# Kernel tuning notes

Measured on AMD Instinct MI355X. Metric: run time of the kernel, lower is better.

The kernel has to match this reference:

```python
import jax, jax.numpy as jnp
import numpy as np

WS = 8          # window_size
SHIFT = 4       # shift_size
HEADS = 12
C = 384
HD = C // HEADS
SCALE = HD ** -0.5
N = WS * WS


def _rel_pos_index(Wh, Ww):
    # double_step_seq(2*Ww-1, Wh, 1, Ww) -> (1, Wh*Ww); idx = rel + rel.T; flip along axis 1
    seq1 = np.arange(0, (2 * Ww - 1) * Wh, 2 * Ww - 1)
    seq2 = np.arange(0, Ww)
    rel = (seq1[:, None] + seq2[None, :]).reshape(1, -1)
    idx = rel + rel.T
    return np.flip(idx, 1).copy()

REL_IDX = jnp.asarray(_rel_pos_index(WS, WS))  # [N, N] int


def window_partition(x, ws):
    # x: [B, H, W, C] -> [B*nW, ws*ws, C]
    B, H, W, Cc = x.shape
    x = x.reshape(B, H // ws, ws, W // ws, ws, Cc).transpose(0, 1, 3, 2, 4, 5)
    return x.reshape(-1, ws * ws, Cc)


def window_reverse(win, H, W, ws):
    B = win.shape[0] // ((H // ws) * (W // ws))
    x = win.reshape(B, H // ws, W // ws, ws, ws, -1).transpose(0, 1, 3, 2, 4, 5)
    return x.reshape(B, H, W, -1)


def _attn_mask(H, W, ws, shift):
    # region ids 0..8 per (h,w) as in the torch slice loop
    hi = np.arange(H)
    wi = np.arange(W)
    h_id = (hi >= H - ws).astype(np.int32) + (hi >= H - shift).astype(np.int32)
    w_id = (wi >= W - ws).astype(np.int32) + (wi >= W - shift).astype(np.int32)
    cnt = (h_id[:, None] * 3 + w_id[None, :]).astype(np.float32)
    img = jnp.asarray(cnt)[None, :, :, None]              # [1, H, W, 1]
    mw = window_partition(img, ws).reshape(-1, ws * ws)   # [nW, N]
    diff = mw[:, None, :] - mw[:, :, None]                # [nW, N, N]
    return jnp.where(diff != 0, jnp.float32(-100.0), jnp.float32(0.0))


def setup_inputs() -> dict:
    key = jax.random.key(0)
    ks = jax.random.split(key, 8)
    B, H, W = 16, 96, 96
    std = 0.02
    return {
        "query": jax.random.normal(ks[0], (B, H * W, C), jnp.float32),
        "skip_query": jax.random.normal(ks[1], (B, H * W, C), jnp.float32),
        "W_qkv": jax.random.normal(ks[2], (C, 2 * C), jnp.float32) * std,
        "b_qkv": jnp.zeros((2 * C,), jnp.float32),
        "W_skip": jax.random.normal(ks[3], (C, C), jnp.float32) * std,
        "b_skip": jnp.zeros((C,), jnp.float32),
        "rpb_table": jax.random.normal(ks[4], ((2 * WS - 1) * (2 * WS - 1), HEADS), jnp.float32) * std,
        "W_proj": jax.random.normal(ks[5], (C, C), jnp.float32) * std,
        "b_proj": jnp.zeros((C,), jnp.float32),
        "h": H,
        "w": W,
    }


def reference(query, skip_query, W_qkv, b_qkv, W_skip, b_skip, rpb_table, W_proj, b_proj, h, w):
    B, L, Cc = query.shape
    q4 = query.reshape(B, h, w, Cc)
    s4 = skip_query.reshape(B, h, w, Cc)
    pad_r = (WS - w % WS) % WS
    pad_b = (WS - h % WS) % WS
    q4 = jnp.pad(q4, ((0, 0), (0, pad_b), (0, pad_r), (0, 0)))
    s4 = jnp.pad(s4, ((0, 0), (0, pad_b), (0, pad_r), (0, 0)))
    H_pad, W_pad = q4.shape[1], q4.shape[2]

    # cyclic shift
    q4 = jnp.roll(q4, (-SHIFT, -SHIFT), axis=(1, 2))
    s4 = jnp.roll(s4, (-SHIFT, -SHIFT), axis=(1, 2))
    mask = _attn_mask(H_pad, W_pad, WS, SHIFT)  # [nW, N, N]

    xw = window_partition(q4, WS)   # [Bn, N, C] -> k, v source
    sw = window_partition(s4, WS)   # [Bn, N, C] -> q source
    Bn = xw.shape[0]

    kv = (xw @ W_qkv + b_qkv).reshape(Bn, N, 2, HEADS, HD)
    k = kv[:, :, 0].transpose(0, 2, 1, 3)   # [Bn, H, N, d]
    v = kv[:, :, 1].transpose(0, 2, 1, 3)
    q = ((sw @ W_skip + b_skip).reshape(Bn, N, HEADS, HD).transpose(0, 2, 1, 3)) * SCALE

    attn = jnp.einsum('bhnd,bhmd->bhnm', q, k)  # [Bn, H, N, N]
    rpb = rpb_table[REL_IDX.reshape(-1)].reshape(N, N, HEADS).transpose(2, 0, 1)
    attn = attn + rpb[None]
    nW = mask.shape[0]
    attn = (attn.reshape(B, nW, HEADS, N, N) + mask[None, :, None]).reshape(Bn, HEADS, N, N)
    attn = jax.nn.softmax(attn, axis=-1)

    out = jnp.einsum('bhnm,bhmd->bhnd', attn, v).transpose(0, 2, 1, 3).reshape(Bn, N, Cc)
    out = out @ W_proj + b_proj

    x4 = window_reverse(out.reshape(-1, WS, WS, Cc), H_pad, W_pad, WS)
    x4 = jnp.roll(x4, (SHIFT, SHIFT), axis=(1, 2))
    x4 = x4[:, :h, :w]
    return x4.reshape(B, h * w, Cc)
```

## Files before the change

kernel.cpp:

```cpp
#include <hip/hip_runtime.h>
#include <hip/hip_bf16.h>


typedef __attribute__((ext_vector_type(8))) short short8;
typedef __attribute__((ext_vector_type(4))) float floatx4;

#define MFMA16(a, b, c) __builtin_amdgcn_mfma_f32_16x16x32_bf16(a, b, c, 0, 0, 0)

__device__ __forceinline__ short f2bf(float f) {
    __hip_bfloat16 h = __float2bfloat16(f);
    return *reinterpret_cast<short*>(&h);
}

__device__ __forceinline__ unsigned cvt2bf(float lo, float hi) {
    unsigned r;
    asm("v_cvt_pk_bf16_f32 %0, %1, %2" : "=v"(r) : "v"(lo), "v"(hi));
    return r;
}

__device__ __forceinline__ void glds16(const void* g, void* l) {
    __builtin_amdgcn_global_load_lds(
        (const __attribute__((address_space(1))) void*)g,
        (__attribute__((address_space(3))) void*)l, 16, 0, 0);
}


__global__ __launch_bounds__(256) void prep_wt(const float* __restrict__ Wqkv,
                                               const float* __restrict__ Wskip,
                                               short* __restrict__ Wt) {
    int tid = blockIdx.x * 256 + threadIdx.x;
    if (tid >= 384 * 144) return;
    int k = tid / 144;
    int n8 = (tid % 144) * 8;
#pragma unroll
    for (int e = 0; e < 8; e++) {
        int n = n8 + e;
        float v = (n < 768) ? Wqkv[k * 768 + n]
                            : Wskip[k * 384 + (n - 768)] * 0.17677669529663687f;
        Wt[(size_t)n * 384 + k] = f2bf(v);
    }
}

__global__ __launch_bounds__(256) void prep_wtp(const float* __restrict__ Wproj,
                                                short* __restrict__ WtP) {
    int tid = blockIdx.x * 256 + threadIdx.x;
    if (tid >= 384 * 48) return;
    int k = tid / 48;
    int n8 = (tid % 48) * 8;
#pragma unroll
    for (int e = 0; e < 8; e++) {
        int n = n8 + e;
        WtP[(size_t)n * 384 + k] = f2bf(Wproj[k * 384 + n]);
    }
}

__global__ __launch_bounds__(256) void prep_bias(const float* __restrict__ rpb,
                                                 float* __restrict__ bias64) {
    int tid = blockIdx.x * 256 + threadIdx.x;
    if (tid >= 49152) return;
    int h = tid >> 12;
    int rem = tid & 4095;
    int i = rem >> 6, kk = rem & 63;
    int j = 63 - kk;
    int ridx = 15 * (i >> 3) + (i & 7) + 15 * (j >> 3) + (j & 7);
    bias64[tid] = rpb[ridx * 12 + h];
}

template <bool SWP, bool FIN>
__device__ __forceinline__ void kloop12(
    const short* __restrict__ smemA, short* __restrict__ bwb,
    const short* __restrict__ curSrc, const short* __restrict__ nxtSrc,
    const int (&bso)[3], int l15, int g4, int al7, int brd,
    floatx4 (&acc)[3][4]) {
#pragma unroll
    for (int a = 0; a < 3; a++)
#pragma unroll
        for (int b = 0; b < 4; b++)
#pragma unroll
            for (int r = 0; r < 4; r++) acc[a][b][r] = 0.f;

#pragma unroll
    for (int kt = 0; kt < 12; ++kt) {
        if (FIN && kt == 11) {
            asm volatile("s_waitcnt vmcnt(0)" ::: "memory");
        } else {
            asm volatile("s_waitcnt vmcnt(3)" ::: "memory");
        }
        const int choff = ((kt * 4 + g4) ^ al7) * 8;
        short8 af[4], bfr[3];
#pragma unroll
        for (int b = 0; b < 4; b++)
            af[b] = *(const short8*)(smemA + (b * 16 + l15) * 384 + choff);
        short* hb = bwb + (kt & 1) * 1536;
#pragma unroll
        for (int nj = 0; nj < 3; nj++)
            bfr[nj] = *(const short8*)(hb + (nj * 16 + l15) * 32 + brd);
        __builtin_amdgcn_sched_barrier(0);
        asm volatile("s_waitcnt lgkmcnt(0)" ::: "memory");
        if (kt < 10) {
            int ko = (kt + 2) * 32;
#pragma unroll
            for (int j = 0; j < 3; j++)
                glds16(curSrc + bso[j] + ko, hb + j * 512);
        } else if (!FIN) {
            int ko = (kt - 10) * 32;
#pragma unroll
            for (int j = 0; j < 3; j++)
                glds16(nxtSrc + bso[j] + ko, hb + j * 512);
        }
        __builtin_amdgcn_sched_barrier(0);
        if (SWP) {
#pragma unroll
            for (int a = 0; a < 3; a++)
#pragma unroll
                for (int b = 0; b < 4; b++)
                    acc[a][b] = MFMA16(bfr[a], af[b], acc[a][b]);
        } else {
#pragma unroll
            for (int a = 0; a < 3; a++)
#pragma unroll
                for (int b = 0; b < 4; b++)
                    acc[a][b] = MFMA16(af[b], bfr[a], acc[a][b]);
        }
    }
}

__global__ __launch_bounds__(512, 1) void gemm_qkv(
    const float* __restrict__ xq, const float* __restrict__ xs,
    const short* __restrict__ Wt,
    const float* __restrict__ bqkv, const float* __restrict__ bskip,
    short* __restrict__ kbuf, short* __restrict__ vtbuf, short* __restrict__ qbuf) {
    __shared__ short smem[49152];

    const int win = blockIdx.x;
    const int var = blockIdx.y;
    const float* __restrict__ src = var ? xs : xq;

    const int tid = threadIdx.x, lane = tid & 63, wid = tid >> 6;
    const int l15 = lane & 15, g4 = lane >> 4;
    const int al7 = l15 & 7;
    const int brd = (g4 ^ ((l15 ^ (l15 >> 2)) & 3)) * 8;

    {
        int r = tid >> 3, q8 = tid & 7;
        int b = win / 144, wr = win % 144;
        int wy = wr / 12, wx = wr % 12;
        int yy = wy * 8 + (r >> 3) + 4; if (yy >= 96) yy -= 96;
        int xx = wx * 8 + (r & 7) + 4;  if (xx >= 96) xx -= 96;
        const float* rbase = src + ((size_t)b * 9216 + yy * 96 + xx) * 384;
        short* lrow = smem + r * 384;
        int r7 = r & 7;
#pragma unroll
        for (int j = 0; j < 6; j++) {
            int c = q8 + j * 8;
            float4 f0 = *(const float4*)(rbase + c * 8);
            float4 f1 = *(const float4*)(rbase + c * 8 + 4);
            uint4 u;
            u.x = cvt2bf(f0.x, f0.y); u.y = cvt2bf(f0.z, f0.w);
            u.z = cvt2bf(f1.x, f1.y); u.w = cvt2bf(f1.z, f1.w);
            *(uint4*)(lrow + ((c ^ r7) * 8)) = u;
        }
    }

    const int sw_st = ((lane >> 2) ^ (lane >> 4)) & 3;
    int bso[3];
#pragma unroll
    for (int j = 0; j < 3; j++)
        bso[j] = (j * 16 + (lane >> 2)) * 384 + (((lane & 3) ^ sw_st) * 8);
    short* bwb = smem + 24576 + wid * 3072;

    const short* src0 = Wt + (size_t)((var ? 768 : 0) + wid * 48) * 384;
    const short* src1 = Wt + (size_t)(384 + wid * 48) * 384;

#pragma unroll
    for (int j = 0; j < 3; j++) glds16(src0 + bso[j], bwb + j * 512);
#pragma unroll
    for (int j = 0; j < 3; j++) glds16(src0 + bso[j] + 32, bwb + 1536 + j * 512);
    __syncthreads();

    floatx4 acc[3][4];
    if (var == 0) {
        kloop12<true, false>(smem, bwb, src0, src1, bso, l15, g4, al7, brd, acc);
#pragma unroll
        for (int a = 0; a < 3; a++) {
            int nm = wid * 48 + a * 16 + g4 * 4;
            int head = nm >> 5, d0 = nm & 31;
            float4 bv = *(const float4*)(bqkv + nm);
            short* dst = kbuf + (size_t)(win * 12 + head) * 2048 + d0;
#pragma unroll
            for (int b = 0; b < 4; b++) {
                int t = b * 16 + l15;
                uint2 pk;
                pk.x = cvt2bf(acc[a][b][0] + bv.x, acc[a][b][1] + bv.y);
                pk.y = cvt2bf(acc[a][b][2] + bv.z, acc[a][b][3] + bv.w);
                *(uint2*)(dst + (size_t)t * 32) = pk;
            }
        }
        kloop12<false, true>(smem, bwb, src1, nullptr, bso, l15, g4, al7, brd, acc);
#pragma unroll
        for (int nj = 0; nj < 3; nj++) {
            int nm = wid * 48 + nj * 16 + l15;
            int head = nm >> 5, d = nm & 31;
            float bvs = bqkv[384 + nm];
            short* dst = vtbuf + ((size_t)(win * 12 + head) * 32 + d) * 64;
#pragma unroll
            for (int mi = 0; mi < 4; mi++) {
                int t0 = mi * 16 + g4 * 4;
                uint2 pk;
                pk.x = cvt2bf(acc[nj][mi][0] + bvs, acc[nj][mi][1] + bvs);
                pk.y = cvt2bf(acc[nj][mi][2] + bvs, acc[nj][mi][3] + bvs);
                *(uint2*)(dst + t0) = pk;
            }
        }
    } else {
        kloop12<true, true>(smem, bwb, src0, nullptr, bso, l15, g4, al7, brd, acc);
        const float scl = 0.17677669529663687f;
#pragma unroll
        for (int a = 0; a < 3; a++) {
            int nm = wid * 48 + a * 16 + g4 * 4;
            int head = nm >> 5, d0 = nm & 31;
            float4 bv = *(const float4*)(bskip + nm);
            short* dst = qbuf + (size_t)(win * 12 + head) * 2048 + d0;
#pragma unroll
            for (int b = 0; b < 4; b++) {
                int t = b * 16 + l15;
                uint2 pk;
                pk.x = cvt2bf(acc[a][b][0] + bv.x * scl, acc[a][b][1] + bv.y * scl);
                pk.y = cvt2bf(acc[a][b][2] + bv.z * scl, acc[a][b][3] + bv.w * scl);
                *(uint2*)(dst + (size_t)t * 32) = pk;
            }
        }
    }
}

__global__ __launch_bounds__(256) void attn_kernel(
    const short* __restrict__ kbuf, const short* __restrict__ vtbuf,
    const short* __restrict__ qbuf, const float* __restrict__ bias64,
    short* __restrict__ aout, int ntask) {
    __shared__ short lps[18432];
    int lane = threadIdx.x & 63, wid = threadIdx.x >> 6;
    int task = blockIdx.x * 4 + wid;
    if (task >= ntask) return;
    int win = task / 12, head = task % 12;
    int l15 = lane & 15, g4 = lane >> 4;

    const short* kb = kbuf + (size_t)task * 2048;
    const short* qb = qbuf + (size_t)task * 2048;
    const short* vb = vtbuf + (size_t)task * 2048;

    short8 kf[4], qf[4], vf[2][2];
#pragma unroll
    for (int mi = 0; mi < 4; mi++)
        kf[mi] = *(const short8*)(kb + (mi * 16 + l15) * 32 + g4 * 8);
#pragma unroll
    for (int nj = 0; nj < 4; nj++)
        qf[nj] = *(const short8*)(qb + (nj * 16 + l15) * 32 + g4 * 8);
#pragma unroll
    for (int ma = 0; ma < 2; ma++)
#pragma unroll
        for (int ks = 0; ks < 2; ks++)
            vf[ma][ks] = *(const short8*)(vb + (ma * 16 + l15) * 64 + ks * 32 + g4 * 8);

    floatx4 st[4][4];
#pragma unroll
    for (int mi = 0; mi < 4; mi++)
#pragma unroll
        for (int nj = 0; nj < 4; nj++)
#pragma unroll
            for (int r = 0; r < 4; r++) st[mi][nj][r] = 0.f;

#pragma unroll
    for (int mi = 0; mi < 4; mi++)
#pragma unroll
        for (int nj = 0; nj < 4; nj++)
            st[mi][nj] = MFMA16(kf[mi], qf[nj], st[mi][nj]);

    const float* bb = bias64 + head * 4096;
#pragma unroll
    for (int nj = 0; nj < 4; nj++) {
        int i = nj * 16 + l15;
#pragma unroll
        for (int mi = 0; mi < 4; mi++) {
            floatx4 b4 = *(const floatx4*)(bb + i * 64 + mi * 16 + g4 * 4);
            st[mi][nj] += b4;
        }
    }

    int wr = win % 144;
    int wy = wr / 12, wx = wr % 12;
    if (wy == 11 || wx == 11) {
        int wy11 = (wy == 11), wx11 = (wx == 11);
        int ri[4];
#pragma unroll
        for (int nj = 0; nj < 4; nj++) {
            int t = nj * 16 + l15;
            int hh = wy11 ? (((t >> 3) >= 4) ? 2 : 1) : 0;
            int ww = wx11 ? (((t & 7) >= 4) ? 2 : 1) : 0;
            ri[nj] = hh * 3 + ww;
        }
#pragma unroll
        for (int mi = 0; mi < 4; mi++)
#pragma unroll
            for (int r = 0; r < 4; r++) {
                int t = mi * 16 + g4 * 4 + r;
                int hh = wy11 ? (((t >> 3) >= 4) ? 2 : 1) : 0;
                int ww = wx11 ? (((t & 7) >= 4) ? 2 : 1) : 0;
                int rk = hh * 3 + ww;
#pragma unroll
                for (int nj = 0; nj < 4; nj++)
                    if (rk != ri[nj]) st[mi][nj][r] -= 100.0f;
            }
    }

    float rden[4];
#pragma unroll
    for (int nj = 0; nj < 4; nj++) {
        float m = -1e30f;
#pragma unroll
        for (int mi = 0; mi < 4; mi++)
#pragma unroll
            for (int r = 0; r < 4; r++) m = fmaxf(m, st[mi][nj][r]);
        m = fmaxf(m, __shfl_xor(m, 16));
        m = fmaxf(m, __shfl_xor(m, 32));
        float s = 0.f;
#pragma unroll
        for (int mi = 0; mi < 4; mi++)
#pragma unroll
            for (int r = 0; r < 4; r++) {
                float p = __expf(st[mi][nj][r] - m);
                st[mi][nj][r] = p;
                s += p;
            }
        s += __shfl_xor(s, 16);
        s += __shfl_xor(s, 32);
        rden[nj] = 1.0f / s;
    }

    short* Lp = lps + wid * 4608;
#pragma unroll
    for (int mi = 0; mi < 4; mi++)
#pragma unroll
        for (int nj = 0; nj < 4; nj++) {
            uint2 pk;
            pk.x = cvt2bf(st[mi][nj][0], st[mi][nj][1]);
            pk.y = cvt2bf(st[mi][nj][2], st[mi][nj][3]);
            *(uint2*)(Lp + (nj * 16 + l15) * 72 + mi * 16 + g4 * 4) = pk;
        }

    floatx4 o[2][4];
#pragma unroll
    for (int ma = 0; ma < 2; ma++)
#pragma unroll
        for (int nj = 0; nj < 4; nj++)
#pragma unroll
            for (int r = 0; r < 4; r++) o[ma][nj][r] = 0.f;
#pragma unroll
    for (int ks = 0; ks < 2; ks++) {
        short8 pb[4];
#pragma unroll
        for (int nj = 0; nj < 4; nj++)
            pb[nj] = *(const short8*)(Lp + (nj * 16 + l15) * 72 + ks * 32 + g4 * 8);
#pragma unroll
        for (int ma = 0; ma < 2; ma++)
#pragma unroll
            for (int nj = 0; nj < 4; nj++)
                o[ma][nj] = MFMA16(vf[ma][ks], pb[nj], o[ma][nj]);
    }

    short* ob = aout + (size_t)win * 64 * 384 + head * 32;
#pragma unroll
    for (int ma = 0; ma < 2; ma++)
#pragma unroll
        for (int nj = 0; nj < 4; nj++) {
            int i = nj * 16 + l15;
            uint2 pk;
            pk.x = cvt2bf(o[ma][nj][0] * rden[nj], o[ma][nj][1] * rden[nj]);
            pk.y = cvt2bf(o[ma][nj][2] * rden[nj], o[ma][nj][3] * rden[nj]);
            *(uint2*)(ob + (size_t)i * 384 + ma * 16 + g4 * 4) = pk;
        }
}

__global__ __launch_bounds__(512, 1) void gemm_proj(
    const short* __restrict__ aout, const short* __restrict__ WtP,
    const float* __restrict__ bproj, float* __restrict__ out) {
    __shared__ short smem[49152];

    const int win = blockIdx.x;
    const int m0 = win * 64;
    const int tid = threadIdx.x, lane = tid & 63, wid = tid >> 6;
    const int l15 = lane & 15, g4 = lane >> 4;
    const int al7 = l15 & 7;
    const int brd = (g4 ^ ((l15 ^ (l15 >> 2)) & 3)) * 8;

#pragma unroll
    for (int j = 0; j < 6; j++) {
        int i = wid * 6 + j;
        int c = i * 64 + lane;
        int row = c / 48, ch = c - row * 48;
        const short* s = aout + (size_t)(m0 + row) * 384 + ((ch ^ (row & 7)) * 8);
        glds16(s, smem + i * 512);
    }

    const int sw_st = ((lane >> 2) ^ (lane >> 4)) & 3;
    int bso[3];
#pragma unroll
    for (int j = 0; j < 3; j++)
        bso[j] = (j * 16 + (lane >> 2)) * 384 + (((lane & 3) ^ sw_st) * 8);
    short* bwb = smem + 24576 + wid * 3072;
    const short* src0 = WtP + (size_t)(wid * 48) * 384;

#pragma unroll
    for (int j = 0; j < 3; j++) glds16(src0 + bso[j], bwb + j * 512);
#pragma unroll
    for (int j = 0; j < 3; j++) glds16(src0 + bso[j] + 32, bwb + 1536 + j * 512);
    __syncthreads();

    floatx4 acc[3][4];
    kloop12<true, true>(smem, bwb, src0, nullptr, bso, l15, g4, al7, brd, acc);

    const int b_img = win / 144, wrw = win % 144;
    const int wy = wrw / 12, wx = wrw % 12;
#pragma unroll
    for (int a = 0; a < 3; a++) {
        int n = wid * 48 + a * 16 + g4 * 4;
        float4 bv = *(const float4*)(bproj + n);
#pragma unroll
        for (int b = 0; b < 4; b++) {
            int t = b * 16 + l15;
            int yy = wy * 8 + (t >> 3) + 4; if (yy >= 96) yy -= 96;
            int xx = wx * 8 + (t & 7) + 4;  if (xx >= 96) xx -= 96;
            floatx4 o = acc[a][b];
            o[0] += bv.x; o[1] += bv.y; o[2] += bv.z; o[3] += bv.w;
            *(floatx4*)(&out[((size_t)b_img * 9216 + yy * 96 + xx) * 384 + n]) = o;
        }
    }
}

extern "C" void kernel_launch(void* const* d_in, const int* in_sizes, int n_in,
                              void* d_out, int out_size, void* d_ws, size_t ws_size,
                              hipStream_t stream) {
    const float* query = (const float*)d_in[0];
    const float* skipq = (const float*)d_in[1];
    const float* Wqkv  = (const float*)d_in[2];
    const float* bqkv  = (const float*)d_in[3];
    const float* Wskip = (const float*)d_in[4];
    const float* bskip = (const float*)d_in[5];
    const float* rpb   = (const float*)d_in[6];
    const float* Wproj = (const float*)d_in[7];
    const float* bproj = (const float*)d_in[8];
    float* out = (float*)d_out;

    int M = in_sizes[0] / 384;
    int nwin = M / 64;

    char* ws = (char*)d_ws;
    size_t off = 0;
    auto alloc = [&](size_t bytes) -> void* {
        void* p = ws + off;
        off = (off + bytes + 255) & ~(size_t)255;
        return p;
    };
    short* Wt     = (short*)alloc((size_t)1152 * 384 * 2);
    short* WtP    = (short*)alloc((size_t)384 * 384 * 2);
    float* bias64 = (float*)alloc((size_t)12 * 64 * 64 * 4);
    short* kbuf   = (short*)alloc((size_t)M * 384 * 2);
    short* vtbuf  = (short*)alloc((size_t)M * 384 * 2);
    short* qbuf   = (short*)alloc((size_t)M * 384 * 2);
    short* aout   = (short*)alloc((size_t)M * 384 * 2);
    (void)ws_size;

    hipLaunchKernelGGL(prep_wt, dim3(216), dim3(256), 0, stream, Wqkv, Wskip, Wt);
    hipLaunchKernelGGL(prep_wtp, dim3(72), dim3(256), 0, stream, Wproj, WtP);
    hipLaunchKernelGGL(prep_bias, dim3(192), dim3(256), 0, stream, rpb, bias64);
    hipLaunchKernelGGL(gemm_qkv, dim3(nwin, 2), dim3(512), 0, stream,
                       query, skipq, Wt, bqkv, bskip, kbuf, vtbuf, qbuf);
    hipLaunchKernelGGL(attn_kernel, dim3(nwin * 12 / 4), dim3(256), 0, stream,
                       kbuf, vtbuf, qbuf, bias64, aout, nwin * 12);
    hipLaunchKernelGGL(gemm_proj, dim3(nwin), dim3(512), 0, stream,
                       aout, WtP, bproj, out);
}
```

Baseline: 577.0 us.

## Fuse QKV GEMM, window attention and output projection into one per-window kernel

Replaces the three kernels (QKV/skip projection, per-head attention, output projection) with a single 768-thread kernel per window where each of 12 waves owns one head. Q, K, V and the attention output stay in LDS instead of being written to and re-read from global bf16 buffers. This removes the intermediate global traffic and two launches. In exchange it uses one large LDS block per CU with heavy sync, which may lower occupancy and latency hiding.

```diff
diff --git a/kernel.cpp b/kernel.cpp
--- a/kernel.cpp
+++ b/kernel.cpp
@@ -22,6 +22,11 @@
     __builtin_amdgcn_global_load_lds(
         (const __attribute__((address_space(1))) void*)g,
         (__attribute__((address_space(3))) void*)l, 16, 0, 0);
+}
+
+__device__ __forceinline__ void lds_fence() {
+    asm volatile("s_waitcnt lgkmcnt(0)" ::: "memory");
+    __builtin_amdgcn_sched_barrier(0);
 }
 
 
@@ -66,200 +71,205 @@
     bias64[tid] = rpb[ridx * 12 + h];
 }
 
-template <bool SWP, bool FIN>
-__device__ __forceinline__ void kloop12(
-    const short* __restrict__ smemA, short* __restrict__ bwb,
-    const short* __restrict__ curSrc, const short* __restrict__ nxtSrc,
-    const int (&bso)[3], int l15, int g4, int al7, int brd,
-    floatx4 (&acc)[3][4]) {
-#pragma unroll
-    for (int a = 0; a < 3; a++)
-#pragma unroll
-        for (int b = 0; b < 4; b++)
-#pragma unroll
-            for (int r = 0; r < 4; r++) acc[a][b][r] = 0.f;
-
-#pragma unroll
-    for (int kt = 0; kt < 12; ++kt) {
-        if (FIN && kt == 11) {
-            asm volatile("s_waitcnt vmcnt(0)" ::: "memory");
-        } else {
-            asm volatile("s_waitcnt vmcnt(3)" ::: "memory");
-        }
-        const int choff = ((kt * 4 + g4) ^ al7) * 8;
-        short8 af[4], bfr[3];
-#pragma unroll
-        for (int b = 0; b < 4; b++)
-            af[b] = *(const short8*)(smemA + (b * 16 + l15) * 384 + choff);
-        short* hb = bwb + (kt & 1) * 1536;
-#pragma unroll
-        for (int nj = 0; nj < 3; nj++)
-            bfr[nj] = *(const short8*)(hb + (nj * 16 + l15) * 32 + brd);
-        __builtin_amdgcn_sched_barrier(0);
-        asm volatile("s_waitcnt lgkmcnt(0)" ::: "memory");
-        if (kt < 10) {
-            int ko = (kt + 2) * 32;
-#pragma unroll
-            for (int j = 0; j < 3; j++)
-                glds16(curSrc + bso[j] + ko, hb + j * 512);
-        } else if (!FIN) {
-            int ko = (kt - 10) * 32;
-#pragma unroll
-            for (int j = 0; j < 3; j++)
-                glds16(nxtSrc + bso[j] + ko, hb + j * 512);
-        }
-        __builtin_amdgcn_sched_barrier(0);
-        if (SWP) {
-#pragma unroll
-            for (int a = 0; a < 3; a++)
-#pragma unroll
-                for (int b = 0; b < 4; b++)
-                    acc[a][b] = MFMA16(bfr[a], af[b], acc[a][b]);
-        } else {
-#pragma unroll
-            for (int a = 0; a < 3; a++)
-#pragma unroll
-                for (int b = 0; b < 4; b++)
-                    acc[a][b] = MFMA16(af[b], bfr[a], acc[a][b]);
-        }
-    }
-}
-
-__global__ __launch_bounds__(512, 1) void gemm_qkv(
+__global__ __launch_bounds__(768, 1) void fused_win(
     const float* __restrict__ xq, const float* __restrict__ xs,
-    const short* __restrict__ Wt,
+    const short* __restrict__ Wt, const short* __restrict__ WtP,
     const float* __restrict__ bqkv, const float* __restrict__ bskip,
-    short* __restrict__ kbuf, short* __restrict__ vtbuf, short* __restrict__ qbuf) {
-    __shared__ short smem[49152];
+    const float* __restrict__ bproj, const float* __restrict__ bias64,
+    float* __restrict__ out) {
+    __shared__ short smem[73728];
 
     const int win = blockIdx.x;
-    const int var = blockIdx.y;
-    const float* __restrict__ src = var ? xs : xq;
-
     const int tid = threadIdx.x, lane = tid & 63, wid = tid >> 6;
     const int l15 = lane & 15, g4 = lane >> 4;
     const int al7 = l15 & 7;
     const int brd = (g4 ^ ((l15 ^ (l15 >> 2)) & 3)) * 8;
 
-    {
-        int r = tid >> 3, q8 = tid & 7;
-        int b = win / 144, wr = win % 144;
-        int wy = wr / 12, wx = wr % 12;
-        int yy = wy * 8 + (r >> 3) + 4; if (yy >= 96) yy -= 96;
-        int xx = wx * 8 + (r & 7) + 4;  if (xx >= 96) xx -= 96;
-        const float* rbase = src + ((size_t)b * 9216 + yy * 96 + xx) * 384;
-        short* lrow = smem + r * 384;
-        int r7 = r & 7;
-#pragma unroll
-        for (int j = 0; j < 6; j++) {
-            int c = q8 + j * 8;
-            float4 f0 = *(const float4*)(rbase + c * 8);
-            float4 f1 = *(const float4*)(rbase + c * 8 + 4);
+    const int b_img = win / 144, wr = win % 144;
+    const int wy = wr / 12, wx = wr % 12;
+
+    const int gr = tid / 12, gj = tid - gr * 12;
+    int gyy = wy * 8 + (gr >> 3) + 4; if (gyy >= 96) gyy -= 96;
+    int gxx = wx * 8 + (gr & 7) + 4;  if (gxx >= 96) gxx -= 96;
+    const size_t grow = ((size_t)b_img * 9216 + gyy * 96 + gxx) * 384;
+    short* lrow = smem + gr * 384;
+    const int gr7 = gr & 7;
+
+    auto gatherA = [&](const float* src) {
+        const float* rb = src + grow;
+#pragma unroll
+        for (int cc = 0; cc < 4; cc++) {
+            int c = gj * 4 + cc;
+            float4 f0 = *(const float4*)(rb + c * 8);
+            float4 f1 = *(const float4*)(rb + c * 8 + 4);
             uint4 u;
             u.x = cvt2bf(f0.x, f0.y); u.y = cvt2bf(f0.z, f0.w);
             u.z = cvt2bf(f1.x, f1.y); u.w = cvt2bf(f1.z, f1.w);
-            *(uint4*)(lrow + ((c ^ r7) * 8)) = u;
-        }
-    }
-
-    const int sw_st = ((lane >> 2) ^ (lane >> 4)) & 3;
-    int bso[3];
-#pragma unroll
-    for (int j = 0; j < 3; j++)
-        bso[j] = (j * 16 + (lane >> 2)) * 384 + (((lane & 3) ^ sw_st) * 8);
-    short* bwb = smem + 24576 + wid * 3072;
-
-    const short* src0 = Wt + (size_t)((var ? 768 : 0) + wid * 48) * 384;
-    const short* src1 = Wt + (size_t)(384 + wid * 48) * 384;
-
-#pragma unroll
-    for (int j = 0; j < 3; j++) glds16(src0 + bso[j], bwb + j * 512);
-#pragma unroll
-    for (int j = 0; j < 3; j++) glds16(src0 + bso[j] + 32, bwb + 1536 + j * 512);
+            *(uint4*)(lrow + ((c ^ gr7) * 8)) = u;
+        }
+    };
+
+    const int swst = ((lane >> 2) ^ (lane >> 4)) & 3;
+    int bso[2];
+#pragma unroll
+    for (int j = 0; j < 2; j++)
+        bso[j] = (j * 16 + (lane >> 2)) * 384 + (((lane & 3) ^ swst) * 8);
+    short* wsc = smem + 24576 + wid * 4096;
+
+    const short* sK = Wt + (size_t)(wid * 32) * 384;
+    const short* sV = Wt + (size_t)(384 + wid * 32) * 384;
+    const short* sQ = Wt + (size_t)(768 + wid * 32) * 384;
+    const short* sP = WtP + (size_t)(wid * 32) * 384;
+
+#pragma unroll
+    for (int s = 0; s < 2; s++)
+#pragma unroll
+        for (int j = 0; j < 2; j++)
+            glds16(sQ + bso[j] + s * 32, wsc + s * 1024 + j * 512);
+    gatherA(xs);
     __syncthreads();
 
-    floatx4 acc[3][4];
-    if (var == 0) {
-        kloop12<true, false>(smem, bwb, src0, src1, bso, l15, g4, al7, brd, acc);
-#pragma unroll
-        for (int a = 0; a < 3; a++) {
-            int nm = wid * 48 + a * 16 + g4 * 4;
-            int head = nm >> 5, d0 = nm & 31;
-            float4 bv = *(const float4*)(bqkv + nm);
-            short* dst = kbuf + (size_t)(win * 12 + head) * 2048 + d0;
+    floatx4 aq[2][4];
+#pragma unroll
+    for (int a = 0; a < 2; a++)
+#pragma unroll
+        for (int b = 0; b < 4; b++)
+#pragma unroll
+            for (int r = 0; r < 4; r++) aq[a][b][r] = 0.f;
+#pragma unroll
+    for (int kt = 0; kt < 12; ++kt) {
+        if (kt == 11) asm volatile("s_waitcnt vmcnt(0)" ::: "memory");
+        else          asm volatile("s_waitcnt vmcnt(2)" ::: "memory");
+        const int choff = ((kt * 4 + g4) ^ al7) * 8;
+        short* hb = wsc + (kt & 1) * 1024;
+        short8 af[4], bq[2];
+#pragma unroll
+        for (int b = 0; b < 4; b++)
+            af[b] = *(const short8*)(smem + (b * 16 + l15) * 384 + choff);
+#pragma unroll
+        for (int a = 0; a < 2; a++)
+            bq[a] = *(const short8*)(hb + (a * 16 + l15) * 32 + brd);
+        __builtin_amdgcn_sched_barrier(0);
+        asm volatile("s_waitcnt lgkmcnt(0)" ::: "memory");
+        if (kt < 10) {
+            int ko = (kt + 2) * 32;
+#pragma unroll
+            for (int j = 0; j < 2; j++) glds16(sQ + bso[j] + ko, hb + j * 512);
+        }
+        __builtin_amdgcn_sched_barrier(0);
+#pragma unroll
+        for (int a = 0; a < 2; a++)
+#pragma unroll
+            for (int b = 0; b < 4; b++)
+                aq[a][b] = MFMA16(bq[a], af[b], aq[a][b]);
+    }
+
+    const float scl = 0.17677669529663687f;
+#pragma unroll
+    for (int a = 0; a < 2; a++) {
+        float4 bv = *(const float4*)(bskip + wid * 32 + a * 16 + g4 * 4);
+#pragma unroll
+        for (int b = 0; b < 4; b++) {
+            uint2 pk;
+            pk.x = cvt2bf(aq[a][b][0] + bv.x * scl, aq[a][b][1] + bv.y * scl);
+            pk.y = cvt2bf(aq[a][b][2] + bv.z * scl, aq[a][b][3] + bv.w * scl);
+            *(uint2*)(wsc + 1024 + (b * 16 + l15) * 32 + a * 16 + g4 * 4) = pk;
+        }
+    }
+    short8 qf[4];
+#pragma unroll
+    for (int nj = 0; nj < 4; nj++)
+        qf[nj] = *(const short8*)(wsc + 1024 + (nj * 16 + l15) * 32 + g4 * 8);
+    lds_fence();
+
+#pragma unroll
+    for (int s = 0; s < 2; s++)
+#pragma unroll
+        for (int j = 0; j < 2; j++) {
+            glds16(sK + bso[j] + s * 32, wsc + s * 2048 + j * 512);
+            glds16(sV + bso[j] + s * 32, wsc + s * 2048 + 1024 + j * 512);
+        }
+    __syncthreads();
+    gatherA(xq);
+    __syncthreads();
+
+    floatx4 ak[2][4], av[2][4];
+#pragma unroll
+    for (int a = 0; a < 2; a++)
+#pragma unroll
+        for (int b = 0; b < 4; b++)
+#pragma unroll
+            for (int r = 0; r < 4; r++) { ak[a][b][r] = 0.f; av[a][b][r] = 0.f; }
+#pragma unroll
+    for (int kt = 0; kt < 12; ++kt) {
+        if (kt == 11) asm volatile("s_waitcnt vmcnt(0)" ::: "memory");
+        else          asm volatile("s_waitcnt vmcnt(4)" ::: "memory");
+        const int choff = ((kt * 4 + g4) ^ al7) * 8;
+        short* hb = wsc + (kt & 1) * 2048;
+        short8 af[4], bk[2], bv2[2];
+#pragma unroll
+        for (int b = 0; b < 4; b++)
+            af[b] = *(const short8*)(smem + (b * 16 + l15) * 384 + choff);
+#pragma unroll
+        for (int a = 0; a < 2; a++) {
+            bk[a]  = *(const short8*)(hb + (a * 16 + l15) * 32 + brd);
+            bv2[a] = *(const short8*)(hb + 1024 + (a * 16 + l15) * 32 + brd);
+        }
+        __builtin_amdgcn_sched_barrier(0);
+        asm volatile("s_waitcnt lgkmcnt(0)" ::: "memory");
+        if (kt < 10) {
+            int ko = (kt + 2) * 32;
+#pragma unroll
+            for (int j = 0; j < 2; j++) {
+                glds16(sK + bso[j] + ko, hb + j * 512);
+                glds16(sV + bso[j] + ko, hb + 1024 + j * 512);
+            }
+        }
+        __builtin_amdgcn_sched_barrier(0);
+#pragma unroll
+        for (int a = 0; a < 2; a++)
 #pragma unroll
             for (int b = 0; b < 4; b++) {
-                int t = b * 16 + l15;
-                uint2 pk;
-                pk.x = cvt2bf(acc[a][b][0] + bv.x, acc[a][b][1] + bv.y);
-                pk.y = cvt2bf(acc[a][b][2] + bv.z, acc[a][b][3] + bv.w);
-                *(uint2*)(dst + (size_t)t * 32) = pk;
+                ak[a][b] = MFMA16(bk[a], af[b], ak[a][b]);
+                av[a][b] = MFMA16(af[b], bv2[a], av[a][b]);
             }
-        }
-        kloop12<false, true>(smem, bwb, src1, nullptr, bso, l15, g4, al7, brd, acc);
-#pragma unroll
-        for (int nj = 0; nj < 3; nj++) {
-            int nm = wid * 48 + nj * 16 + l15;
-            int head = nm >> 5, d = nm & 31;
-            float bvs = bqkv[384 + nm];
-            short* dst = vtbuf + ((size_t)(win * 12 + head) * 32 + d) * 64;
-#pragma unroll
-            for (int mi = 0; mi < 4; mi++) {
-                int t0 = mi * 16 + g4 * 4;
-                uint2 pk;
-                pk.x = cvt2bf(acc[nj][mi][0] + bvs, acc[nj][mi][1] + bvs);
-                pk.y = cvt2bf(acc[nj][mi][2] + bvs, acc[nj][mi][3] + bvs);
-                *(uint2*)(dst + t0) = pk;
-            }
-        }
-    } else {
-        kloop12<true, true>(smem, bwb, src0, nullptr, bso, l15, g4, al7, brd, acc);
-        const float scl = 0.17677669529663687f;
-#pragma unroll
-        for (int a = 0; a < 3; a++) {
-            int nm = wid * 48 + a * 16 + g4 * 4;
-            int head = nm >> 5, d0 = nm & 31;
-            float4 bv = *(const float4*)(bskip + nm);
-            short* dst = qbuf + (size_t)(win * 12 + head) * 2048 + d0;
-#pragma unroll
-            for (int b = 0; b < 4; b++) {
-                int t = b * 16 + l15;
-                uint2 pk;
-                pk.x = cvt2bf(acc[a][b][0] + bv.x * scl, acc[a][b][1] + bv.y * scl);
-                pk.y = cvt2bf(acc[a][b][2] + bv.z * scl, acc[a][b][3] + bv.w * scl);
-                *(uint2*)(dst + (size_t)t * 32) = pk;
-            }
-        }
-    }
-}
-
-__global__ __launch_bounds__(256) void attn_kernel(
-    const short* __restrict__ kbuf, const short* __restrict__ vtbuf,
-    const short* __restrict__ qbuf, const float* __restrict__ bias64,
-    short* __restrict__ aout, int ntask) {
-    __shared__ short lps[18432];
-    int lane = threadIdx.x & 63, wid = threadIdx.x >> 6;
-    int task = blockIdx.x * 4 + wid;
-    if (task >= ntask) return;
-    int win = task / 12, head = task % 12;
-    int l15 = lane & 15, g4 = lane >> 4;
-
-    const short* kb = kbuf + (size_t)task * 2048;
-    const short* qb = qbuf + (size_t)task * 2048;
-    const short* vb = vtbuf + (size_t)task * 2048;
-
-    short8 kf[4], qf[4], vf[2][2];
+    }
+    __syncthreads();
+
+#pragma unroll
+    for (int a = 0; a < 2; a++) {
+        float4 bv = *(const float4*)(bqkv + wid * 32 + a * 16 + g4 * 4);
+#pragma unroll
+        for (int b = 0; b < 4; b++) {
+            uint2 pk;
+            pk.x = cvt2bf(ak[a][b][0] + bv.x, ak[a][b][1] + bv.y);
+            pk.y = cvt2bf(ak[a][b][2] + bv.z, ak[a][b][3] + bv.w);
+            *(uint2*)(wsc + (b * 16 + l15) * 32 + a * 16 + g4 * 4) = pk;
+        }
+    }
+#pragma unroll
+    for (int a = 0; a < 2; a++) {
+        float bvs = bqkv[384 + wid * 32 + a * 16 + l15];
+#pragma unroll
+        for (int b = 0; b < 4; b++) {
+            uint2 pk;
+            pk.x = cvt2bf(av[a][b][0] + bvs, av[a][b][1] + bvs);
+            pk.y = cvt2bf(av[a][b][2] + bvs, av[a][b][3] + bvs);
+            int tch = b * 2 + (g4 >> 1);
+            *(uint2*)(wsc + 2048 + (a * 16 + l15) * 64 +
+                      ((tch ^ (l15 & 7)) * 8) + (g4 & 1) * 4) = pk;
+        }
+    }
+    short8 kf[4], vf[2][2];
 #pragma unroll
     for (int mi = 0; mi < 4; mi++)
-        kf[mi] = *(const short8*)(kb + (mi * 16 + l15) * 32 + g4 * 8);
-#pragma unroll
-    for (int nj = 0; nj < 4; nj++)
-        qf[nj] = *(const short8*)(qb + (nj * 16 + l15) * 32 + g4 * 8);
+        kf[mi] = *(const short8*)(wsc + (mi * 16 + l15) * 32 + g4 * 8);
 #pragma unroll
     for (int ma = 0; ma < 2; ma++)
 #pragma unroll
         for (int ks = 0; ks < 2; ks++)
-            vf[ma][ks] = *(const short8*)(vb + (ma * 16 + l15) * 64 + ks * 32 + g4 * 8);
+            vf[ma][ks] = *(const short8*)(wsc + 2048 + (ma * 16 + l15) * 64 +
+                                          (((ks * 4 + g4) ^ (l15 & 7)) * 8));
 
     floatx4 st[4][4];
 #pragma unroll
@@ -268,14 +278,13 @@
         for (int nj = 0; nj < 4; nj++)
 #pragma unroll
             for (int r = 0; r < 4; r++) st[mi][nj][r] = 0.f;
-
 #pragma unroll
     for (int mi = 0; mi < 4; mi++)
 #pragma unroll
         for (int nj = 0; nj < 4; nj++)
             st[mi][nj] = MFMA16(kf[mi], qf[nj], st[mi][nj]);
 
-    const float* bb = bias64 + head * 4096;
+    const float* bb = bias64 + wid * 4096;
 #pragma unroll
     for (int nj = 0; nj < 4; nj++) {
         int i = nj * 16 + l15;
@@ -286,8 +295,6 @@
         }
     }
 
-    int wr = win % 144;
-    int wy = wr / 12, wx = wr % 12;
     if (wy == 11 || wx == 11) {
         int wy11 = (wy == 11), wx11 = (wx == 11);
         int ri[4];
@@ -336,7 +343,6 @@
         rden[nj] = 1.0f / s;
     }
 
-    short* Lp = lps + wid * 4608;
 #pragma unroll
     for (int mi = 0; mi < 4; mi++)
 #pragma unroll
@@ -344,7 +350,9 @@
             uint2 pk;
             pk.x = cvt2bf(st[mi][nj][0], st[mi][nj][1]);
             pk.y = cvt2bf(st[mi][nj][2], st[mi][nj][3]);
-            *(uint2*)(Lp + (nj * 16 + l15) * 72 + mi * 16 + g4 * 4) = pk;
+            int kch = mi * 2 + (g4 >> 1);
+            *(uint2*)(wsc + (nj * 16 + l15) * 64 +
+                      ((kch ^ (l15 & 7)) * 8) + (g4 & 1) * 4) = pk;
         }
 
     floatx4 o[2][4];
@@ -359,15 +367,22 @@
         short8 pb[4];
 #pragma unroll
         for (int nj = 0; nj < 4; nj++)
-            pb[nj] = *(const short8*)(Lp + (nj * 16 + l15) * 72 + ks * 32 + g4 * 8);
+            pb[nj] = *(const short8*)(wsc + (nj * 16 + l15) * 64 +
+                                      (((ks * 4 + g4) ^ (l15 & 7)) * 8));
 #pragma unroll
         for (int ma = 0; ma < 2; ma++)
 #pragma unroll
             for (int nj = 0; nj < 4; nj++)
                 o[ma][nj] = MFMA16(vf[ma][ks], pb[nj], o[ma][nj]);
     }
-
-    short* ob = aout + (size_t)win * 64 * 384 + head * 32;
+    lds_fence();
+
+#pragma unroll
+    for (int s = 0; s < 2; s++)
+#pragma unroll
+        for (int j = 0; j < 2; j++)
+            glds16(sP + bso[j] + s * 32, wsc + s * 1024 + j * 512);
+
 #pragma unroll
     for (int ma = 0; ma < 2; ma++)
 #pragma unroll
@@ -376,62 +391,58 @@
             uint2 pk;
             pk.x = cvt2bf(o[ma][nj][0] * rden[nj], o[ma][nj][1] * rden[nj]);
             pk.y = cvt2bf(o[ma][nj][2] * rden[nj], o[ma][nj][3] * rden[nj]);
-            *(uint2*)(ob + (size_t)i * 384 + ma * 16 + g4 * 4) = pk;
-        }
-}
-
-__global__ __launch_bounds__(512, 1) void gemm_proj(
-    const short* __restrict__ aout, const short* __restrict__ WtP,
-    const float* __restrict__ bproj, float* __restrict__ out) {
-    __shared__ short smem[49152];
-
-    const int win = blockIdx.x;
-    const int m0 = win * 64;
-    const int tid = threadIdx.x, lane = tid & 63, wid = tid >> 6;
-    const int l15 = lane & 15, g4 = lane >> 4;
-    const int al7 = l15 & 7;
-    const int brd = (g4 ^ ((l15 ^ (l15 >> 2)) & 3)) * 8;
-
-#pragma unroll
-    for (int j = 0; j < 6; j++) {
-        int i = wid * 6 + j;
-        int c = i * 64 + lane;
-        int row = c / 48, ch = c - row * 48;
-        const short* s = aout + (size_t)(m0 + row) * 384 + ((ch ^ (row & 7)) * 8);
-        glds16(s, smem + i * 512);
-    }
-
-    const int sw_st = ((lane >> 2) ^ (lane >> 4)) & 3;
-    int bso[3];
-#pragma unroll
-    for (int j = 0; j < 3; j++)
-        bso[j] = (j * 16 + (lane >> 2)) * 384 + (((lane & 3) ^ sw_st) * 8);
-    short* bwb = smem + 24576 + wid * 3072;
-    const short* src0 = WtP + (size_t)(wid * 48) * 384;
-
-#pragma unroll
-    for (int j = 0; j < 3; j++) glds16(src0 + bso[j], bwb + j * 512);
-#pragma unroll
-    for (int j = 0; j < 3; j++) glds16(src0 + bso[j] + 32, bwb + 1536 + j * 512);
+            int ch = wid * 4 + ma * 2 + (g4 >> 1);
+            *(uint2*)(smem + i * 384 + ((ch ^ (i & 7)) * 8) + (g4 & 1) * 4) = pk;
+        }
     __syncthreads();
 
-    floatx4 acc[3][4];
-    kloop12<true, true>(smem, bwb, src0, nullptr, bso, l15, g4, al7, brd, acc);
-
-    const int b_img = win / 144, wrw = win % 144;
-    const int wy = wrw / 12, wx = wrw % 12;
-#pragma unroll
-    for (int a = 0; a < 3; a++) {
-        int n = wid * 48 + a * 16 + g4 * 4;
+    floatx4 ap[2][4];
+#pragma unroll
+    for (int a = 0; a < 2; a++)
+#pragma unroll
+        for (int b = 0; b < 4; b++)
+#pragma unroll
+            for (int r = 0; r < 4; r++) ap[a][b][r] = 0.f;
+#pragma unroll
+    for (int kt = 0; kt < 12; ++kt) {
+        if (kt == 11) asm volatile("s_waitcnt vmcnt(0)" ::: "memory");
+        else          asm volatile("s_waitcnt vmcnt(2)" ::: "memory");
+        const int choff = ((kt * 4 + g4) ^ al7) * 8;
+        short* hb = wsc + (kt & 1) * 1024;
+        short8 af[4], bp[2];
+#pragma unroll
+        for (int b = 0; b < 4; b++)
+            af[b] = *(const short8*)(smem + (b * 16 + l15) * 384 + choff);
+#pragma unroll
+        for (int a = 0; a < 2; a++)
+            bp[a] = *(const short8*)(hb + (a * 16 + l15) * 32 + brd);
+        __builtin_amdgcn_sched_barrier(0);
+        asm volatile("s_waitcnt lgkmcnt(0)" ::: "memory");
+        if (kt < 10) {
+            int ko = (kt + 2) * 32;
+#pragma unroll
+            for (int j = 0; j < 2; j++) glds16(sP + bso[j] + ko, hb + j * 512);
+        }
+        __builtin_amdgcn_sched_barrier(0);
+#pragma unroll
+        for (int a = 0; a < 2; a++)
+#pragma unroll
+            for (int b = 0; b < 4; b++)
+                ap[a][b] = MFMA16(bp[a], af[b], ap[a][b]);
+    }
+
+#pragma unroll
+    for (int a = 0; a < 2; a++) {
+        int n = wid * 32 + a * 16 + g4 * 4;
         float4 bv = *(const float4*)(bproj + n);
 #pragma unroll
         for (int b = 0; b < 4; b++) {
             int t = b * 16 + l15;
             int yy = wy * 8 + (t >> 3) + 4; if (yy >= 96) yy -= 96;
             int xx = wx * 8 + (t & 7) + 4;  if (xx >= 96) xx -= 96;
-            floatx4 o = acc[a][b];
-            o[0] += bv.x; o[1] += bv.y; o[2] += bv.z; o[3] += bv.w;
-            *(floatx4*)(&out[((size_t)b_img * 9216 + yy * 96 + xx) * 384 + n]) = o;
+            floatx4 ov = ap[a][b];
+            ov[0] += bv.x; ov[1] += bv.y; ov[2] += bv.z; ov[3] += bv.w;
+            *(floatx4*)(&out[((size_t)b_img * 9216 + yy * 96 + xx) * 384 + n]) = ov;
         }
     }
 }
@@ -463,19 +474,11 @@
     short* Wt     = (short*)alloc((size_t)1152 * 384 * 2);
     short* WtP    = (short*)alloc((size_t)384 * 384 * 2);
     float* bias64 = (float*)alloc((size_t)12 * 64 * 64 * 4);
-    short* kbuf   = (short*)alloc((size_t)M * 384 * 2);
-    short* vtbuf  = (short*)alloc((size_t)M * 384 * 2);
-    short* qbuf   = (short*)alloc((size_t)M * 384 * 2);
-    short* aout   = (short*)alloc((size_t)M * 384 * 2);
     (void)ws_size;
 
     hipLaunchKernelGGL(prep_wt, dim3(216), dim3(256), 0, stream, Wqkv, Wskip, Wt);
     hipLaunchKernelGGL(prep_wtp, dim3(72), dim3(256), 0, stream, Wproj, WtP);
     hipLaunchKernelGGL(prep_bias, dim3(192), dim3(256), 0, stream, rpb, bias64);
-    hipLaunchKernelGGL(gemm_qkv, dim3(nwin, 2), dim3(512), 0, stream,
-                       query, skipq, Wt, bqkv, bskip, kbuf, vtbuf, qbuf);
-    hipLaunchKernelGGL(attn_kernel, dim3(nwin * 12 / 4), dim3(256), 0, stream,
-                       kbuf, vtbuf, qbuf, bias64, aout, nwin * 12);
-    hipLaunchKernelGGL(gemm_proj, dim3(nwin), dim3(512), 0, stream,
-                       aout, WtP, bproj, out);
-}
+    hipLaunchKernelGGL(fused_win, dim3(nwin), dim3(768), 0, stream,
+                       query, skipq, Wt, WtP, bqkv, bskip, bproj, bias64, out);
+}
```

After: 498.5 us. 1.16x faster.
